# Kernel optimization log

Measured on AMD Instinct MI355X. Metric: run time of the kernel, lower is better.

## Reference

```python
import jax, jax.numpy as jnp
import numpy as np

N = 100000      # number of nodes
E = 1600000     # number of (directed) edges, avg degree 16
DIN = 128       # in_features
DOUT = 32       # out_features
SLOPE = 0.2     # leaky relu negative slope


def setup_inputs() -> dict:
    key = jax.random.key(0)
    k1, k2, k3, k4, k5, k6 = jax.random.split(key, 6)
    x = jax.random.normal(k1, (N, DIN), dtype=jnp.float32)
    edge_index = jax.random.randint(k2, (2, E), 0, N, dtype=jnp.int32)
    # W1 (shared with W2 and used as the feature-update matrix W, 'source' mode)
    W1_w = jax.random.normal(k3, (DOUT, DIN), dtype=jnp.float32) / np.float32(np.sqrt(DIN))
    W1_b = jax.random.normal(k4, (DOUT,), dtype=jnp.float32) * 0.01
    a1_w = jax.random.normal(k5, (DOUT,), dtype=jnp.float32) / np.float32(np.sqrt(DOUT))
    a2_w = jax.random.normal(k6, (DOUT,), dtype=jnp.float32) / np.float32(np.sqrt(DOUT))
    return {"x": x, "edge_index": edge_index, "W1_w": W1_w, "W1_b": W1_b,
            "a1_w": a1_w, "a2_w": a2_w}


def reference(x, edge_index, W1_w, W1_b, a1_w, a2_w):
    n = x.shape[0]
    # append self-loops, as in _sparse_attention
    loops = jnp.arange(n, dtype=edge_index.dtype)
    src = jnp.concatenate([edge_index[0], loops])   # rows  (softmax segments)
    dst = jnp.concatenate([edge_index[1], loops])   # cols
    # h = W1(x) (linear, with bias); W2 = W1 (weight sharing), W = W2 ('source')
    h = x @ W1_w.T + W1_b                           # [N, DOUT]
    z = jax.nn.leaky_relu(h, SLOPE)                 # x1 == x2 under weight sharing
    s1 = z @ a1_w                                   # [N] per-node src score
    s2 = z @ a2_w                                   # [N] per-node dst score
    logits = s1[src] + s2[dst]                      # [E+N] per-edge attention logit
    # row-wise (dim=1) sparse softmax == segment softmax over src
    m = jax.ops.segment_max(logits, src, num_segments=n)
    ex = jnp.exp(logits - m[src])
    denom = jax.ops.segment_sum(ex, src, num_segments=n)
    alpha = ex / denom[src]                         # normalized attention per edge
    # sparse-dense matmul: out[i] = sum_{(i,j)} alpha_ij * h[j]
    return jax.ops.segment_sum(alpha[:, None] * h[dst], src, num_segments=n)
```

## Files before the change

kernel.cpp:

```cpp
#include <hip/hip_runtime.h>
#include <hip/hip_fp16.h>

#define DIN 128
#define DOUT 32
#define SLOPE 0.2f

#define BSHIFT 7
#define BNODES 128
#define NBMAX  800
#define CAP    3072
#define TILE   2048
#define EPB    (TILE / 256)

typedef short s16x8 __attribute__((ext_vector_type(8)));
typedef float f32x4 __attribute__((ext_vector_type(4)));

__device__ __forceinline__ short f2bf(float f) {
    unsigned u = __float_as_uint(f);
    return (short)((u + 0x7fffu + ((u >> 16) & 1u)) >> 16);
}
__device__ __forceinline__ float bf2f(short s) {
    return __uint_as_float(((unsigned)(unsigned short)s) << 16);
}

__device__ __forceinline__ void linear_role(
    int tile, int ntiles, int lane, int N,
    const float* __restrict__ x, const float* __restrict__ W,
    const float* __restrict__ b, const float* __restrict__ a2,
    __half* __restrict__ g16, float* __restrict__ es2)
{
    if (tile >= ntiles) return;
    int m = lane & 15, oct = lane >> 4;
    long rowbase = (long)tile * 16;

    s16x8 bh[2][4], bl[2][4];
    #pragma unroll
    for (int t = 0; t < 2; ++t) {
        const float* wrow = W + (long)(t * 16 + m) * DIN + oct * 8;
        #pragma unroll
        for (int kc = 0; kc < 4; ++kc) {
            float4 w0 = *(const float4*)(wrow + kc * 32);
            float4 w1 = *(const float4*)(wrow + kc * 32 + 4);
            float wf[8] = {w0.x, w0.y, w0.z, w0.w, w1.x, w1.y, w1.z, w1.w};
            #pragma unroll
            for (int j = 0; j < 8; ++j) {
                short hh = f2bf(wf[j]);
                bh[t][kc][j] = hh;
                bl[t][kc][j] = f2bf(wf[j] - bf2f(hh));
            }
        }
    }

    long lrow = rowbase + m; if (lrow > N - 1) lrow = N - 1;
    const float* xrow = x + lrow * DIN + oct * 8;
    f32x4 acc0 = {0.f, 0.f, 0.f, 0.f}, acc1 = {0.f, 0.f, 0.f, 0.f};
    #pragma unroll
    for (int kc = 0; kc < 4; ++kc) {
        float4 x0 = *(const float4*)(xrow + kc * 32);
        float4 x1 = *(const float4*)(xrow + kc * 32 + 4);
        float xf[8] = {x0.x, x0.y, x0.z, x0.w, x1.x, x1.y, x1.z, x1.w};
        s16x8 ah, al;
        #pragma unroll
        for (int j = 0; j < 8; ++j) {
            short hh = f2bf(xf[j]);
            ah[j] = hh;
            al[j] = f2bf(xf[j] - bf2f(hh));
        }
        acc0 = __builtin_amdgcn_mfma_f32_16x16x32_bf16(al, bh[0][kc], acc0, 0, 0, 0);
        acc0 = __builtin_amdgcn_mfma_f32_16x16x32_bf16(ah, bl[0][kc], acc0, 0, 0, 0);
        acc0 = __builtin_amdgcn_mfma_f32_16x16x32_bf16(ah, bh[0][kc], acc0, 0, 0, 0);
        acc1 = __builtin_amdgcn_mfma_f32_16x16x32_bf16(al, bh[1][kc], acc1, 0, 0, 0);
        acc1 = __builtin_amdgcn_mfma_f32_16x16x32_bf16(ah, bl[1][kc], acc1, 0, 0, 0);
        acc1 = __builtin_amdgcn_mfma_f32_16x16x32_bf16(ah, bh[1][kc], acc1, 0, 0, 0);
    }

    int c0 = m, c1 = 16 + m;
    float b0 = b[c0], b1 = b[c1], A0 = a2[c0], A1 = a2[c1];
    float hv0[4], hv1[4], sp[4];
    #pragma unroll
    for (int i = 0; i < 4; ++i) {
        hv0[i] = acc0[i] + b0;
        hv1[i] = acc1[i] + b1;
        float z0 = hv0[i] > 0.f ? hv0[i] : SLOPE * hv0[i];
        float z1 = hv1[i] > 0.f ? hv1[i] : SLOPE * hv1[i];
        sp[i] = z0 * A0 + z1 * A1;
    }
    #pragma unroll
    for (int off = 1; off <= 8; off <<= 1) {
        #pragma unroll
        for (int i = 0; i < 4; ++i) sp[i] += __shfl_xor(sp[i], off, 64);
    }
    #pragma unroll
    for (int i = 0; i < 4; ++i) {
        long r = rowbase + oct * 4 + i;
        if (r >= N) continue;
        float ev = __expf(sp[i]);
        g16[r * DOUT + c0] = __float2half(ev * hv0[i]);
        g16[r * DOUT + c1] = __float2half(ev * hv1[i]);
        if (m == 0) es2[r] = ev;
    }
}

__global__ __launch_bounds__(256) void gat_fused(
    const float* __restrict__ x, const float* __restrict__ W,
    const float* __restrict__ b, const float* __restrict__ a2,
    const int* __restrict__ src, const int* __restrict__ dst,
    __half* __restrict__ g16, float* __restrict__ es2,
    unsigned* __restrict__ ebuf, int* __restrict__ gcursor,
    int N, int E, int ntiles, int nbin, int NB)
{
    if ((int)blockIdx.x >= nbin) {
        int wave = threadIdx.x >> 6;
        int tile = (blockIdx.x - nbin) * 4 + wave;
        linear_role(tile, ntiles, threadIdx.x & 63, N, x, W, b, a2, g16, es2);
        return;
    }
    __shared__ int cnt[NBMAX];
    __shared__ int base[NBMAX];
    int tid = threadIdx.x;
    long tstart = (long)blockIdx.x * TILE;

    for (int i = tid; i < NB; i += 256) cnt[i] = 0;
    __syncthreads();

    int sv[EPB], dv[EPB], rv[EPB];
    #pragma unroll
    for (int it = 0; it < EPB; ++it) {
        long e = tstart + it * 256 + tid;
        int s = (e < E) ? src[e] : -1;
        int d = (e < E) ? dst[e] : 0;
        sv[it] = s;
        dv[it] = d;
        rv[it] = (s >= 0) ? atomicAdd(&cnt[s >> BSHIFT], 1) : 0;
    }
    __syncthreads();
    for (int i = tid; i < NB; i += 256) {
        int c = cnt[i];
        base[i] = c ? atomicAdd(&gcursor[i], c) : 0;
    }
    __syncthreads();
    #pragma unroll
    for (int it = 0; it < EPB; ++it) {
        int s = sv[it];
        if (s >= 0) {
            int bk = s >> BSHIFT;
            int pos = base[bk] + rv[it];
            if (pos < CAP)
                ebuf[(size_t)bk * CAP + pos] =
                    ((unsigned)(s & (BNODES - 1)) << 17) | (unsigned)dv[it];
        }
    }
}

__global__ __launch_bounds__(512) void gat_aggregate(
    const __half* __restrict__ g16, const float* __restrict__ es2,
    const unsigned* __restrict__ ebuf, const int* __restrict__ gcursor,
    float* __restrict__ out, int N)
{
    __shared__ unsigned rs[CAP];
    __shared__ unsigned srt[CAP];
    __shared__ int cnt[BNODES];
    __shared__ int sc[BNODES];
    __shared__ int basep[BNODES];
    __shared__ int pos2[BNODES];
    int tid = threadIdx.x;
    int bk = blockIdx.x;
    int cntb = gcursor[bk]; if (cntb > CAP) cntb = CAP;

    if (tid < BNODES) { cnt[tid] = 0; pos2[tid] = 0; }
    __syncthreads();
    for (int r = tid; r < cntb; r += 512) {
        unsigned u = ebuf[(size_t)bk * CAP + r];
        rs[r] = u;
        atomicAdd(&cnt[u >> 17], 1);
    }
    __syncthreads();
    if (tid < BNODES) sc[tid] = cnt[tid];
    __syncthreads();
    #pragma unroll
    for (int off = 1; off < BNODES; off <<= 1) {
        int t = (tid >= off && tid < BNODES) ? sc[tid - off] : 0;
        __syncthreads();
        if (tid < BNODES) sc[tid] += t;
        __syncthreads();
    }
    if (tid < BNODES) basep[tid] = sc[tid] - cnt[tid];
    __syncthreads();
    for (int r = tid; r < cntb; r += 512) {
        unsigned u = rs[r];
        int sl = (int)(u >> 17);
        int p = basep[sl] + atomicAdd(&pos2[sl], 1);
        srt[p] = u & 0x1FFFFu;
    }
    __syncthreads();

    int unit = tid >> 5, col = tid & 31;
    for (int sl = unit; sl < BNODES; sl += 16) {
        long node = (long)bk * BNODES + sl;
        if (node >= N) break;
        float acc = __half2float(g16[node * DOUT + col]);
        float d = es2[node];
        int e = basep[sl], e_end = basep[sl] + cnt[sl];

        while (e + 8 <= e_end) {
            int dn[8];
            #pragma unroll
            for (int j = 0; j < 8; ++j) dn[j] = (int)srt[e + j];
            unsigned short gv[8];
            #pragma unroll
            for (int j = 0; j < 8; ++j)
                gv[j] = *(const unsigned short*)&g16[(long)dn[j] * DOUT + col];
            float ev[8];
            #pragma unroll
            for (int j = 0; j < 8; ++j) ev[j] = es2[dn[j]];
            #pragma unroll
            for (int j = 0; j < 8; ++j) {
                acc += __half2float(*(const __half*)&gv[j]);
                d += ev[j];
            }
            e += 8;
        }
        while (e + 4 <= e_end) {
            int dn[4];
            #pragma unroll
            for (int j = 0; j < 4; ++j) dn[j] = (int)srt[e + j];
            unsigned short gv[4];
            #pragma unroll
            for (int j = 0; j < 4; ++j)
                gv[j] = *(const unsigned short*)&g16[(long)dn[j] * DOUT + col];
            float ev[4];
            #pragma unroll
            for (int j = 0; j < 4; ++j) ev[j] = es2[dn[j]];
            #pragma unroll
            for (int j = 0; j < 4; ++j) {
                acc += __half2float(*(const __half*)&gv[j]);
                d += ev[j];
            }
            e += 4;
        }
        for (; e < e_end; ++e) {
            int dn = (int)srt[e];
            acc += __half2float(g16[(long)dn * DOUT + col]);
            d += es2[dn];
        }
        out[node * DOUT + col] = acc / d;
    }
}

extern "C" void kernel_launch(void* const* d_in, const int* in_sizes, int n_in,
                              void* d_out, int out_size, void* d_ws, size_t ws_size,
                              hipStream_t stream)
{
    const float* x  = (const float*)d_in[0];
    const int*   ei = (const int*)d_in[1];
    const float* W  = (const float*)d_in[2];
    const float* b  = (const float*)d_in[3];
    const float* a2 = (const float*)d_in[5];
    float* out = (float*)d_out;

    int N = in_sizes[0] / DIN;
    int E = in_sizes[1] / 2;
    const int* src = ei;
    const int* dst = ei + E;

    int NB = (N + BNODES - 1) >> BSHIFT;

    char* ws = (char*)d_ws;
    __half*   g16     = (__half*)ws;   ws += (size_t)N * DOUT * sizeof(__half);
    float*    es2     = (float*)ws;    ws += (size_t)N * sizeof(float);
    int*      gcursor = (int*)ws;      ws += (size_t)NBMAX * sizeof(int);
    unsigned* ebuf    = (unsigned*)ws; ws += (size_t)NB * CAP * sizeof(unsigned);

    int ntiles = (N + 15) / 16;
    int nlin   = (ntiles + 3) / 4;
    int nbin   = (E + TILE - 1) / TILE;

    hipMemsetAsync(gcursor, 0, (size_t)NBMAX * sizeof(int), stream);
    gat_fused    <<<nbin + nlin, 256, 0, stream>>>(x, W, b, a2, src, dst,
                                                   g16, es2, ebuf, gcursor,
                                                   N, E, ntiles, nbin, NB);
    gat_aggregate<<<NB, 512, 0, stream>>>(g16, es2, ebuf, gcursor, out, N);
}
```

Baseline: 176.7 us.

## Split bin cursors into groups and accumulate via LDS atomics instead of sorting

The binning pass now spreads each 128-node bucket across 8 sub-buckets chosen by block index, which cuts contention on the global cursor atomics. Tiles are doubled in size, and each edge record is packed in registers during the first pass. The aggregate kernel no longer sorts edges by local node with a scan. Instead it walks the sub-bucket segments evenly across waves and adds into shared-memory accumulators with LDS atomics. This removes the sort, scan and barrier overhead, at the cost of many shared atomics, a tighter per-group capacity of 384 that could drop edges under skew, and nondeterministic summation order.

```diff
diff --git a/kernel.cpp b/kernel.cpp
--- a/kernel.cpp
+++ b/kernel.cpp
@@ -8,8 +8,9 @@
 #define BSHIFT 7
 #define BNODES 128
 #define NBMAX  800
-#define CAP    3072
-#define TILE   2048
+#define NGRP   8
+#define CAPG   384
+#define TILE   4096
 #define EPB    (TILE / 256)
 
 typedef short s16x8 __attribute__((ext_vector_type(8)));
@@ -118,36 +119,40 @@
     __shared__ int cnt[NBMAX];
     __shared__ int base[NBMAX];
     int tid = threadIdx.x;
+    int grp = blockIdx.x & (NGRP - 1);
     long tstart = (long)blockIdx.x * TILE;
 
     for (int i = tid; i < NB; i += 256) cnt[i] = 0;
     __syncthreads();
 
-    int sv[EPB], dv[EPB], rv[EPB];
+    unsigned rec[EPB];
+    int      bq[EPB];
     #pragma unroll
     for (int it = 0; it < EPB; ++it) {
         long e = tstart + it * 256 + tid;
         int s = (e < E) ? src[e] : -1;
         int d = (e < E) ? dst[e] : 0;
-        sv[it] = s;
-        dv[it] = d;
-        rv[it] = (s >= 0) ? atomicAdd(&cnt[s >> BSHIFT], 1) : 0;
+        if (s >= 0) {
+            int bk = s >> BSHIFT;
+            int rv = atomicAdd(&cnt[bk], 1);
+            rec[it] = ((unsigned)(s & (BNODES - 1)) << 17) | (unsigned)d;
+            bq[it] = (rv < 1023) ? ((bk << 10) | rv) : -1;
+        } else bq[it] = -1;
     }
     __syncthreads();
     for (int i = tid; i < NB; i += 256) {
         int c = cnt[i];
-        base[i] = c ? atomicAdd(&gcursor[i], c) : 0;
+        base[i] = c ? atomicAdd(&gcursor[(i << 3) | grp], c) : 0;
     }
     __syncthreads();
     #pragma unroll
     for (int it = 0; it < EPB; ++it) {
-        int s = sv[it];
-        if (s >= 0) {
-            int bk = s >> BSHIFT;
-            int pos = base[bk] + rv[it];
-            if (pos < CAP)
-                ebuf[(size_t)bk * CAP + pos] =
-                    ((unsigned)(s & (BNODES - 1)) << 17) | (unsigned)dv[it];
+        int q = bq[it];
+        if (q >= 0) {
+            int bk = q >> 10;
+            int pos = base[bk] + (q & 1023);
+            if (pos < CAPG)
+                ebuf[((size_t)((bk << 3) | grp)) * CAPG + pos] = rec[it];
         }
     }
 }
@@ -157,93 +162,64 @@
     const unsigned* __restrict__ ebuf, const int* __restrict__ gcursor,
     float* __restrict__ out, int N)
 {
-    __shared__ unsigned rs[CAP];
-    __shared__ unsigned srt[CAP];
-    __shared__ int cnt[BNODES];
-    __shared__ int sc[BNODES];
-    __shared__ int basep[BNODES];
-    __shared__ int pos2[BNODES];
+    __shared__ float acc[BNODES][DOUT];
+    __shared__ float den[BNODES];
     int tid = threadIdx.x;
     int bk = blockIdx.x;
-    int cntb = gcursor[bk]; if (cntb > CAP) cntb = CAP;
-
-    if (tid < BNODES) { cnt[tid] = 0; pos2[tid] = 0; }
-    __syncthreads();
-    for (int r = tid; r < cntb; r += 512) {
-        unsigned u = ebuf[(size_t)bk * CAP + r];
-        rs[r] = u;
-        atomicAdd(&cnt[u >> 17], 1);
-    }
-    __syncthreads();
-    if (tid < BNODES) sc[tid] = cnt[tid];
-    __syncthreads();
-    #pragma unroll
-    for (int off = 1; off < BNODES; off <<= 1) {
-        int t = (tid >= off && tid < BNODES) ? sc[tid - off] : 0;
-        __syncthreads();
-        if (tid < BNODES) sc[tid] += t;
-        __syncthreads();
-    }
-    if (tid < BNODES) basep[tid] = sc[tid] - cnt[tid];
-    __syncthreads();
-    for (int r = tid; r < cntb; r += 512) {
-        unsigned u = rs[r];
-        int sl = (int)(u >> 17);
-        int p = basep[sl] + atomicAdd(&pos2[sl], 1);
-        srt[p] = u & 0x1FFFFu;
-    }
+
+    for (int i = tid; i < BNODES * DOUT; i += 512) ((float*)acc)[i] = 0.f;
+    if (tid < BNODES) den[tid] = 0.f;
     __syncthreads();
 
     int unit = tid >> 5, col = tid & 31;
+    #pragma unroll 1
+    for (int g = 0; g < NGRP; ++g) {
+        int cg = gcursor[(bk << 3) | g]; if (cg > CAPG) cg = CAPG;
+        const unsigned* seg = ebuf + ((size_t)((bk << 3) | g)) * CAPG;
+        int r    = (cg * unit) >> 4;
+        int rend = (cg * (unit + 1)) >> 4;
+
+        while (r + 8 <= rend) {
+            unsigned uu[8];
+            #pragma unroll
+            for (int j = 0; j < 8; ++j) uu[j] = seg[r + j];
+            int dn[8], sl[8];
+            #pragma unroll
+            for (int j = 0; j < 8; ++j) { dn[j] = (int)(uu[j] & 0x1FFFFu); sl[j] = (int)(uu[j] >> 17); }
+            unsigned short gv[8];
+            #pragma unroll
+            for (int j = 0; j < 8; ++j)
+                gv[j] = *(const unsigned short*)&g16[(long)dn[j] * DOUT + col];
+            float ev[8];
+            if (col == 0) {
+                #pragma unroll
+                for (int j = 0; j < 8; ++j) ev[j] = es2[dn[j]];
+            }
+            #pragma unroll
+            for (int j = 0; j < 8; ++j)
+                atomicAdd(&acc[sl[j]][col], __half2float(*(const __half*)&gv[j]));
+            if (col == 0) {
+                #pragma unroll
+                for (int j = 0; j < 8; ++j) atomicAdd(&den[sl[j]], ev[j]);
+            }
+            r += 8;
+        }
+        for (; r < rend; ++r) {
+            unsigned u = seg[r];
+            int dn = (int)(u & 0x1FFFFu), sl = (int)(u >> 17);
+            float gvf = __half2float(g16[(long)dn * DOUT + col]);
+            atomicAdd(&acc[sl][col], gvf);
+            if (col == 0) atomicAdd(&den[sl], es2[dn]);
+        }
+    }
+    __syncthreads();
+
     for (int sl = unit; sl < BNODES; sl += 16) {
         long node = (long)bk * BNODES + sl;
         if (node >= N) break;
-        float acc = __half2float(g16[node * DOUT + col]);
-        float d = es2[node];
-        int e = basep[sl], e_end = basep[sl] + cnt[sl];
-
-        while (e + 8 <= e_end) {
-            int dn[8];
-            #pragma unroll
-            for (int j = 0; j < 8; ++j) dn[j] = (int)srt[e + j];
-            unsigned short gv[8];
-            #pragma unroll
-            for (int j = 0; j < 8; ++j)
-                gv[j] = *(const unsigned short*)&g16[(long)dn[j] * DOUT + col];
-            float ev[8];
-            #pragma unroll
-            for (int j = 0; j < 8; ++j) ev[j] = es2[dn[j]];
-            #pragma unroll
-            for (int j = 0; j < 8; ++j) {
-                acc += __half2float(*(const __half*)&gv[j]);
-                d += ev[j];
-            }
-            e += 8;
-        }
-        while (e + 4 <= e_end) {
-            int dn[4];
-            #pragma unroll
-            for (int j = 0; j < 4; ++j) dn[j] = (int)srt[e + j];
-            unsigned short gv[4];
-            #pragma unroll
-            for (int j = 0; j < 4; ++j)
-                gv[j] = *(const unsigned short*)&g16[(long)dn[j] * DOUT + col];
-            float ev[4];
-            #pragma unroll
-            for (int j = 0; j < 4; ++j) ev[j] = es2[dn[j]];
-            #pragma unroll
-            for (int j = 0; j < 4; ++j) {
-                acc += __half2float(*(const __half*)&gv[j]);
-                d += ev[j];
-            }
-            e += 4;
-        }
-        for (; e < e_end; ++e) {
-            int dn = (int)srt[e];
-            acc += __half2float(g16[(long)dn * DOUT + col]);
-            d += es2[dn];
-        }
-        out[node * DOUT + col] = acc / d;
+        float self = __half2float(g16[node * DOUT + col]);
+        float dsum = den[sl] + es2[node];
+        out[node * DOUT + col] = (acc[sl][col] + self) / dsum;
     }
 }
 
@@ -268,14 +244,14 @@
     char* ws = (char*)d_ws;
     __half*   g16     = (__half*)ws;   ws += (size_t)N * DOUT * sizeof(__half);
     float*    es2     = (float*)ws;    ws += (size_t)N * sizeof(float);
-    int*      gcursor = (int*)ws;      ws += (size_t)NBMAX * sizeof(int);
-    unsigned* ebuf    = (unsigned*)ws; ws += (size_t)NB * CAP * sizeof(unsigned);
+    int*      gcursor = (int*)ws;      ws += (size_t)NBMAX * NGRP * sizeof(int);
+    unsigned* ebuf    = (unsigned*)ws; ws += (size_t)NB * NGRP * CAPG * sizeof(unsigned);
 
     int ntiles = (N + 15) / 16;
     int nlin   = (ntiles + 3) / 4;
     int nbin   = (E + TILE - 1) / TILE;
 
-    hipMemsetAsync(gcursor, 0, (size_t)NBMAX * sizeof(int), stream);
+    hipMemsetAsync(gcursor, 0, (size_t)NBMAX * NGRP * sizeof(int), stream);
     gat_fused    <<<nbin + nlin, 256, 0, stream>>>(x, W, b, a2, src, dst,
                                                    g16, es2, ebuf, gcursor,
                                                    N, E, ntiles, nbin, NB);
```

Result: slower. 492.5 us (+178.7%).

## Replace global-atomic bucket scatter with per-tile local sort and offset table

Applied to the files above, without the earlier changes.

The binning phase no longer takes global atomic cursors per bucket. Each 4096-edge tile now counts its edges per bucket in shared memory, prefix-scans the counts, writes a per-tile offset table, and scatters its edges contiguously within its own tile slice. This removes the memset and the global atomic contention, and keeps the scatter writes local to one tile. In exchange, the aggregate kernel must read one offset row per tile and gather each bucket's segments with serial per-thread loops over up to 391 tiles. This risks load imbalance and poorly coalesced reads, and it limits the block to 512 tiles and 511 edges per bucket per tile.

```diff
diff --git a/kernel.cpp b/kernel.cpp
--- a/kernel.cpp
+++ b/kernel.cpp
@@ -7,9 +7,10 @@
 
 #define BSHIFT 7
 #define BNODES 128
-#define NBMAX  800
+#define NBS    1024
+#define BPITCH 784
 #define CAP    3072
-#define TILE   2048
+#define TILE   4096
 #define EPB    (TILE / 256)
 
 typedef short s16x8 __attribute__((ext_vector_type(8)));
@@ -106,8 +107,8 @@
     const float* __restrict__ b, const float* __restrict__ a2,
     const int* __restrict__ src, const int* __restrict__ dst,
     __half* __restrict__ g16, float* __restrict__ es2,
-    unsigned* __restrict__ ebuf, int* __restrict__ gcursor,
-    int N, int E, int ntiles, int nbin, int NB)
+    unsigned* __restrict__ ebuf, int* __restrict__ boff,
+    int N, int E, int ntiles, int nbin)
 {
     if ((int)blockIdx.x >= nbin) {
         int wave = threadIdx.x >> 6;
@@ -115,47 +116,74 @@
         linear_role(tile, ntiles, threadIdx.x & 63, N, x, W, b, a2, g16, es2);
         return;
     }
-    __shared__ int cnt[NBMAX];
-    __shared__ int base[NBMAX];
+    __shared__ int cnt[NBS];
+    __shared__ int offs[NBS];
+    __shared__ int wsum[4], wbase[4];
     int tid = threadIdx.x;
     long tstart = (long)blockIdx.x * TILE;
 
-    for (int i = tid; i < NB; i += 256) cnt[i] = 0;
-    __syncthreads();
-
-    int sv[EPB], dv[EPB], rv[EPB];
+    for (int i = tid; i < NBS; i += 256) cnt[i] = 0;
+    __syncthreads();
+
+    unsigned rec[EPB];
+    int      bq[EPB];
     #pragma unroll
     for (int it = 0; it < EPB; ++it) {
         long e = tstart + it * 256 + tid;
         int s = (e < E) ? src[e] : -1;
         int d = (e < E) ? dst[e] : 0;
-        sv[it] = s;
-        dv[it] = d;
-        rv[it] = (s >= 0) ? atomicAdd(&cnt[s >> BSHIFT], 1) : 0;
-    }
-    __syncthreads();
-    for (int i = tid; i < NB; i += 256) {
-        int c = cnt[i];
-        base[i] = c ? atomicAdd(&gcursor[i], c) : 0;
-    }
-    __syncthreads();
-    #pragma unroll
-    for (int it = 0; it < EPB; ++it) {
-        int s = sv[it];
         if (s >= 0) {
             int bk = s >> BSHIFT;
-            int pos = base[bk] + rv[it];
-            if (pos < CAP)
-                ebuf[(size_t)bk * CAP + pos] =
-                    ((unsigned)(s & (BNODES - 1)) << 17) | (unsigned)dv[it];
+            int rv = atomicAdd(&cnt[bk], 1);
+            rec[it] = ((unsigned)(s & (BNODES - 1)) << 17) | (unsigned)d;
+            bq[it] = (rv < 511) ? ((bk << 9) | rv) : -1;
+        } else bq[it] = -1;
+    }
+    __syncthreads();
+
+    int t4 = tid << 2;
+    int c0 = cnt[t4], c1 = cnt[t4 + 1], c2 = cnt[t4 + 2], c3 = cnt[t4 + 3];
+    int s4 = c0 + c1 + c2 + c3;
+    int v = s4;
+    #pragma unroll
+    for (int off = 1; off < 64; off <<= 1) {
+        int t = __shfl_up(v, off, 64);
+        if ((tid & 63) >= off) v += t;
+    }
+    if ((tid & 63) == 63) wsum[tid >> 6] = v;
+    __syncthreads();
+    if (tid == 0) {
+        int a = 0;
+        #pragma unroll
+        for (int w = 0; w < 4; ++w) { wbase[w] = a; a += wsum[w]; }
+    }
+    __syncthreads();
+    int base = wbase[tid >> 6] + (v - s4);
+    offs[t4]     = base;
+    offs[t4 + 1] = base + c0;
+    offs[t4 + 2] = base + c0 + c1;
+    offs[t4 + 3] = base + c0 + c1 + c2;
+    __syncthreads();
+
+    for (int i = tid; i < BPITCH - 1; i += 256)
+        boff[(size_t)blockIdx.x * BPITCH + i] = offs[i];
+    if (tid == 0)
+        boff[(size_t)blockIdx.x * BPITCH + BPITCH - 1] = offs[BPITCH - 1];
+
+    #pragma unroll
+    for (int it = 0; it < EPB; ++it) {
+        int q = bq[it];
+        if (q >= 0) {
+            int pos = offs[q >> 9] + (q & 511);
+            ebuf[tstart + pos] = rec[it];
         }
     }
 }
 
 __global__ __launch_bounds__(512) void gat_aggregate(
     const __half* __restrict__ g16, const float* __restrict__ es2,
-    const unsigned* __restrict__ ebuf, const int* __restrict__ gcursor,
-    float* __restrict__ out, int N)
+    const unsigned* __restrict__ ebuf, const int* __restrict__ boff,
+    float* __restrict__ out, int N, int nbin)
 {
     __shared__ unsigned rs[CAP];
     __shared__ unsigned srt[CAP];
@@ -163,18 +191,48 @@
     __shared__ int sc[BNODES];
     __shared__ int basep[BNODES];
     __shared__ int pos2[BNODES];
+    __shared__ int wsum[8], wbase[8], totsh;
     int tid = threadIdx.x;
     int bk = blockIdx.x;
-    int cntb = gcursor[bk]; if (cntb > CAP) cntb = CAP;
 
     if (tid < BNODES) { cnt[tid] = 0; pos2[tid] = 0; }
     __syncthreads();
-    for (int r = tid; r < cntb; r += 512) {
-        unsigned u = ebuf[(size_t)bk * CAP + r];
-        rs[r] = u;
-        atomicAdd(&cnt[u >> 17], 1);
-    }
-    __syncthreads();
+
+    int rstart = 0, rlen = 0;
+    if (tid < nbin) {
+        const int* row = boff + (size_t)tid * BPITCH;
+        rstart = row[bk];
+        rlen   = row[bk + 1] - rstart;
+    }
+    int v = rlen;
+    #pragma unroll
+    for (int off = 1; off < 64; off <<= 1) {
+        int t = __shfl_up(v, off, 64);
+        if ((tid & 63) >= off) v += t;
+    }
+    if ((tid & 63) == 63) wsum[tid >> 6] = v;
+    __syncthreads();
+    if (tid == 0) {
+        int a = 0;
+        #pragma unroll
+        for (int w = 0; w < 8; ++w) { wbase[w] = a; a += wsum[w]; }
+        totsh = a;
+    }
+    __syncthreads();
+    int dest = wbase[tid >> 6] + (v - rlen);
+    int lim = CAP - dest; if (lim < 0) lim = 0;
+    if (rlen > lim) rlen = lim;
+    {
+        const unsigned* seg = ebuf + (size_t)tid * TILE + rstart;
+        for (int j = 0; j < rlen; ++j) {
+            unsigned u = seg[j];
+            rs[dest + j] = u;
+            atomicAdd(&cnt[u >> 17], 1);
+        }
+    }
+    __syncthreads();
+    int cntb = totsh; if (cntb > CAP) cntb = CAP;
+
     if (tid < BNODES) sc[tid] = cnt[tid];
     __syncthreads();
     #pragma unroll
@@ -264,20 +322,19 @@
     const int* dst = ei + E;
 
     int NB = (N + BNODES - 1) >> BSHIFT;
+    int nbin = (E + TILE - 1) / TILE;
 
     char* ws = (char*)d_ws;
-    __half*   g16     = (__half*)ws;   ws += (size_t)N * DOUT * sizeof(__half);
-    float*    es2     = (float*)ws;    ws += (size_t)N * sizeof(float);
-    int*      gcursor = (int*)ws;      ws += (size_t)NBMAX * sizeof(int);
-    unsigned* ebuf    = (unsigned*)ws; ws += (size_t)NB * CAP * sizeof(unsigned);
+    __half*   g16  = (__half*)ws;   ws += (size_t)N * DOUT * sizeof(__half);
+    float*    es2  = (float*)ws;    ws += (size_t)N * sizeof(float);
+    int*      boff = (int*)ws;      ws += (size_t)nbin * BPITCH * sizeof(int);
+    unsigned* ebuf = (unsigned*)ws; ws += (size_t)nbin * TILE * sizeof(unsigned);
 
     int ntiles = (N + 15) / 16;
     int nlin   = (ntiles + 3) / 4;
-    int nbin   = (E + TILE - 1) / TILE;
-
-    hipMemsetAsync(gcursor, 0, (size_t)NBMAX * sizeof(int), stream);
+
     gat_fused    <<<nbin + nlin, 256, 0, stream>>>(x, W, b, a2, src, dst,
-                                                   g16, es2, ebuf, gcursor,
-                                                   N, E, ntiles, nbin, NB);
-    gat_aggregate<<<NB, 512, 0, stream>>>(g16, es2, ebuf, gcursor, out, N);
-}
+                                                   g16, es2, ebuf, boff,
+                                                   N, E, ntiles, nbin);
+    gat_aggregate<<<NB, 512, 0, stream>>>(g16, es2, ebuf, boff, out, N, nbin);
+}
```

New measurement: 165.7 us. 1.07x faster.
